# Kernel tuning notes

Hardware: AMD Instinct MI355X
Metric: run time of the kernel (lower is better)

Reference implementation:

```python
import jax, jax.numpy as jnp
import numpy as np

D_MODEL = 2048
NUM_EXPERTS = 64
TOP_K = 2


def setup_inputs() -> dict:
    key = jax.random.key(0)
    kx, kw, kb = jax.random.split(key, 3)
    x = jax.random.normal(kx, (4, 4096, D_MODEL), dtype=jnp.float32)
    # nn.Linear default init: U(-1/sqrt(fan_in), 1/sqrt(fan_in))
    bound = 1.0 / np.sqrt(D_MODEL)
    W = jax.random.uniform(kw, (NUM_EXPERTS, D_MODEL), dtype=jnp.float32, minval=-bound, maxval=bound)
    b = jax.random.uniform(kb, (NUM_EXPERTS,), dtype=jnp.float32, minval=-bound, maxval=bound)
    return {"x": x, "W": W, "b": b}


def reference(x, W, b):
    # Router logits: [B, S, E]
    logits = jnp.einsum("bsd,ed->bse", x, W) + b
    # Top-k over expert dim
    max_k, max_k_index = jax.lax.top_k(logits, TOP_K)  # [B,S,K]
    # Scatter top-k logits into -inf background (equivalent to torch scatter
    # since scattered values are the logits themselves at those indices)
    mask = jnp.any(
        max_k_index[..., None] == jnp.arange(NUM_EXPERTS), axis=-2
    )  # [B,S,E] bool
    sparse = jnp.where(mask, logits, -jnp.inf)
    sf = jax.nn.softmax(sparse, axis=-1)
    return sf, max_k_index
```

## Files before the change

kernel.cpp:

```cpp
#include <hip/hip_runtime.h>
#include <hip/hip_bf16.h>
#include <math.h>

constexpr int D      = 2048;
constexpr int NE     = 64;
constexpr int TOKENS = 16384;
constexpr int TPB    = 64;
constexpr int NBLK   = TOKENS / TPB;
constexpr int NWAVE  = 8;
constexpr int KSLICE = D / NWAVE;
constexpr int KC     = 32;
constexpr int NKC    = KSLICE / KC;
constexpr int PAD    = 66;
constexpr int NM     = TPB / 16;

typedef __attribute__((ext_vector_type(8))) short bf16x8;
typedef __attribute__((ext_vector_type(4))) float f32x4;

static __device__ inline unsigned short f2bf_u(float x) {
  __hip_bfloat16 h = __float2bfloat16(x);
  unsigned short u; __builtin_memcpy(&u, &h, 2); return u;
}
static __device__ inline float bfu2f(unsigned short u) {
  __hip_bfloat16 h; __builtin_memcpy(&h, &u, 2);
  return __bfloat162float(h);
}

static __device__ inline void cvt_hilo(const float* f, bf16x8& hi, bf16x8& lo) {
#pragma unroll
  for (int j = 0; j < 8; ++j) {
    unsigned short h = f2bf_u(f[j]);
    float hf = bfu2f(h);
    unsigned short lw = f2bf_u(f[j] - hf);
    hi[j] = (short)h;
    lo[j] = (short)lw;
  }
}

__global__ __launch_bounds__(256)
void prep_w(const float* __restrict__ W, unsigned short* __restrict__ Whi,
            unsigned short* __restrict__ Wlo) {
  const int i = (blockIdx.x * 256 + threadIdx.x) * 4;
  float4 v = *reinterpret_cast<const float4*>(W + i);
  float f[4] = {v.x, v.y, v.z, v.w};
#pragma unroll
  for (int j = 0; j < 4; ++j) {
    unsigned short h = f2bf_u(f[j]);
    float hf = bfu2f(h);
    Whi[i + j] = h;
    Wlo[i + j] = f2bf_u(f[j] - hf);
  }
}

__global__ __launch_bounds__(512, 2)
void router_main(const float* __restrict__ X,
                 const unsigned short* __restrict__ Whi,
                 const unsigned short* __restrict__ Wlo,
                 const float* __restrict__ bias,
                 float* __restrict__ out) {
  __shared__ float red[4][TPB][PAD];
  __shared__ int   i1s[TPB], i2s[TPB];
  __shared__ float p1s[TPB], p2s[TPB];

  const int t  = threadIdx.x;
  const int w  = t >> 6;
  const int l  = t & 63;
  const int lm = l & 15;
  const int lk = l >> 4;
  const int tile = (blockIdx.x & 7) * (NBLK / 8) + (blockIdx.x >> 3);
  const int tok0 = tile * TPB;

  f32x4 acc[NM][4];
#pragma unroll
  for (int m = 0; m < NM; ++m)
#pragma unroll
    for (int n = 0; n < 4; ++n) acc[m][n] = (f32x4){0.f, 0.f, 0.f, 0.f};

  const unsigned short* whp = Whi + (size_t)lm * D + w * KSLICE + lk * 8;
  const unsigned short* wlp = Wlo + (size_t)lm * D + w * KSLICE + lk * 8;
  const float* xr[NM];
#pragma unroll
  for (int m = 0; m < NM; ++m)
    xr[m] = X + (size_t)(tok0 + m * 16 + lm) * D + w * KSLICE + lk * 8;

  float4 c0[NM], c1[NM];
#pragma unroll
  for (int m = 0; m < NM; ++m) {
    c0[m] = *reinterpret_cast<const float4*>(xr[m]);
    c1[m] = *reinterpret_cast<const float4*>(xr[m] + 4);
  }

#pragma unroll
  for (int kc = 0; kc < NKC; ++kc) {
    const int ko = kc * KC;

    bf16x8 bh[4], bl[4];
#pragma unroll
    for (int n = 0; n < 4; ++n) {
      bh[n] = *reinterpret_cast<const bf16x8*>(whp + (size_t)n * 16 * D + ko);
      bl[n] = *reinterpret_cast<const bf16x8*>(wlp + (size_t)n * 16 * D + ko);
    }

    float4 n0[NM], n1[NM];
    if (kc < NKC - 1) {
#pragma unroll
      for (int m = 0; m < NM; ++m) {
        n0[m] = *reinterpret_cast<const float4*>(xr[m] + (kc + 1) * KC);
        n1[m] = *reinterpret_cast<const float4*>(xr[m] + (kc + 1) * KC + 4);
      }
    }

#pragma unroll
    for (int m = 0; m < NM; ++m) {
      float f[8];
      *reinterpret_cast<float4*>(&f[0]) = c0[m];
      *reinterpret_cast<float4*>(&f[4]) = c1[m];
      bf16x8 ah, al;
      cvt_hilo(f, ah, al);
#pragma unroll
      for (int n = 0; n < 4; ++n) {
        acc[m][n] = __builtin_amdgcn_mfma_f32_16x16x32_bf16(ah, bh[n], acc[m][n], 0, 0, 0);
        acc[m][n] = __builtin_amdgcn_mfma_f32_16x16x32_bf16(ah, bl[n], acc[m][n], 0, 0, 0);
        acc[m][n] = __builtin_amdgcn_mfma_f32_16x16x32_bf16(al, bh[n], acc[m][n], 0, 0, 0);
        acc[m][n] = __builtin_amdgcn_mfma_f32_16x16x32_bf16(al, bl[n], acc[m][n], 0, 0, 0);
      }
    }
    if (kc < NKC - 1) {
#pragma unroll
      for (int m = 0; m < NM; ++m) { c0[m] = n0[m]; c1[m] = n1[m]; }
    }
  }

  const int rtok = t >> 3;
  const int re0  = (t & 7) * 8;
  float s[8];

  if (w < 4) {
#pragma unroll
    for (int m = 0; m < NM; ++m)
#pragma unroll
      for (int n = 0; n < 4; ++n)
#pragma unroll
        for (int j = 0; j < 4; ++j)
          red[w][m * 16 + lk * 4 + j][n * 16 + lm] = acc[m][n][j];
  }
  __syncthreads();
#pragma unroll
  for (int q = 0; q < 8; ++q) {
    const int e = re0 + q;
    float v = bias[e];
#pragma unroll
    for (int ww = 0; ww < 4; ++ww) v += red[ww][rtok][e];
    s[q] = v;
  }
  __syncthreads();
  if (w >= 4) {
#pragma unroll
    for (int m = 0; m < NM; ++m)
#pragma unroll
      for (int n = 0; n < 4; ++n)
#pragma unroll
        for (int j = 0; j < 4; ++j)
          red[w - 4][m * 16 + lk * 4 + j][n * 16 + lm] = acc[m][n][j];
  }
  __syncthreads();
#pragma unroll
  for (int q = 0; q < 8; ++q) {
    const int e = re0 + q;
    float v = s[q];
#pragma unroll
    for (int ww = 0; ww < 4; ++ww) v += red[ww][rtok][e];
    red[0][rtok][e] = v;
  }
  __syncthreads();

  if (t < TPB) {
    float m1 = -INFINITY, m2 = -INFINITY;
    int j1 = 0, j2 = 0;
    for (int e = 0; e < NE; ++e) {
      const float v = red[0][t][e];
      if (v > m1) { m2 = m1; j2 = j1; m1 = v; j1 = e; }
      else if (v > m2) { m2 = v; j2 = e; }
    }
    const float e2  = expf(m2 - m1);
    const float inv = 1.0f / (1.0f + e2);
    i1s[t] = j1; i2s[t] = j2;
    p1s[t] = inv; p2s[t] = e2 * inv;
    float* oidx = out + (size_t)TOKENS * NE + (size_t)(tok0 + t) * 2;
    oidx[0] = (float)j1;
    oidx[1] = (float)j2;
  }
  __syncthreads();

  {
    const int tok = t >> 3;
    const int e0  = (t & 7) * 8;
    const int j1 = i1s[tok], j2 = i2s[tok];
    const float pa = p1s[tok], pb2 = p2s[tok];
    float vv[8];
#pragma unroll
    for (int q = 0; q < 8; ++q) {
      const int e = e0 + q;
      vv[q] = (e == j1) ? pa : ((e == j2) ? pb2 : 0.f);
    }
    float* obase = out + (size_t)(tok0 + tok) * NE + e0;
    *reinterpret_cast<float4*>(obase)     = make_float4(vv[0], vv[1], vv[2], vv[3]);
    *reinterpret_cast<float4*>(obase + 4) = make_float4(vv[4], vv[5], vv[6], vv[7]);
  }
}

extern "C" void kernel_launch(void* const* d_in, const int* in_sizes, int n_in,
                              void* d_out, int out_size, void* d_ws, size_t ws_size,
                              hipStream_t stream) {
  const float* X = (const float*)d_in[0];
  const float* W = (const float*)d_in[1];
  const float* B = (const float*)d_in[2];
  float* out = (float*)d_out;

  unsigned short* Whi = (unsigned short*)d_ws;
  unsigned short* Wlo = Whi + (size_t)NE * D;

  prep_w<<<dim3(NE * D / (256 * 4)), dim3(256), 0, stream>>>(W, Whi, Wlo);
  router_main<<<dim3(NBLK), dim3(512), 0, stream>>>(X, Whi, Wlo, B, out);
}
```

Baseline: 47.84 us.

## Split token tiles across two wave groups with 1024-thread blocks

Doubles the block to 16 waves, with each group of 8 K-slice waves handling half of the 64 tokens (two 16-row tiles instead of four). This halves per-thread accumulator and prefetch registers so more waves can be resident, aiming to hide X load latency better. In exchange, each W fragment is now loaded by twice as many waves, adding cache traffic, and the larger blocks may reduce scheduling flexibility.

After: 60.72 us. 26.9% more time.

```diff
diff --git a/kernel.cpp b/kernel.cpp
--- a/kernel.cpp
+++ b/kernel.cpp
@@ -12,7 +12,6 @@
 constexpr int KC     = 32;
 constexpr int NKC    = KSLICE / KC;
 constexpr int PAD    = 66;
-constexpr int NM     = TPB / 16;
 
 typedef __attribute__((ext_vector_type(8))) short bf16x8;
 typedef __attribute__((ext_vector_type(4))) float f32x4;
@@ -52,7 +51,7 @@
   }
 }
 
-__global__ __launch_bounds__(512, 2)
+__global__ __launch_bounds__(1024, 4)
 void router_main(const float* __restrict__ X,
                  const unsigned short* __restrict__ Whi,
                  const unsigned short* __restrict__ Wlo,
@@ -63,29 +62,31 @@
   __shared__ float p1s[TPB], p2s[TPB];
 
   const int t  = threadIdx.x;
-  const int w  = t >> 6;
+  const int wv = t >> 6;
+  const int w  = wv & 7;
+  const int h  = wv >> 3;
   const int l  = t & 63;
   const int lm = l & 15;
   const int lk = l >> 4;
   const int tile = (blockIdx.x & 7) * (NBLK / 8) + (blockIdx.x >> 3);
   const int tok0 = tile * TPB;
 
-  f32x4 acc[NM][4];
-#pragma unroll
-  for (int m = 0; m < NM; ++m)
+  f32x4 acc[2][4];
+#pragma unroll
+  for (int m = 0; m < 2; ++m)
 #pragma unroll
     for (int n = 0; n < 4; ++n) acc[m][n] = (f32x4){0.f, 0.f, 0.f, 0.f};
 
   const unsigned short* whp = Whi + (size_t)lm * D + w * KSLICE + lk * 8;
   const unsigned short* wlp = Wlo + (size_t)lm * D + w * KSLICE + lk * 8;
-  const float* xr[NM];
-#pragma unroll
-  for (int m = 0; m < NM; ++m)
-    xr[m] = X + (size_t)(tok0 + m * 16 + lm) * D + w * KSLICE + lk * 8;
-
-  float4 c0[NM], c1[NM];
-#pragma unroll
-  for (int m = 0; m < NM; ++m) {
+  const float* xr[2];
+#pragma unroll
+  for (int m = 0; m < 2; ++m)
+    xr[m] = X + (size_t)(tok0 + (h * 2 + m) * 16 + lm) * D + w * KSLICE + lk * 8;
+
+  float4 c0[2], c1[2];
+#pragma unroll
+  for (int m = 0; m < 2; ++m) {
     c0[m] = *reinterpret_cast<const float4*>(xr[m]);
     c1[m] = *reinterpret_cast<const float4*>(xr[m] + 4);
   }
@@ -101,17 +102,17 @@
       bl[n] = *reinterpret_cast<const bf16x8*>(wlp + (size_t)n * 16 * D + ko);
     }
 
-    float4 n0[NM], n1[NM];
+    float4 n0[2], n1[2];
     if (kc < NKC - 1) {
 #pragma unroll
-      for (int m = 0; m < NM; ++m) {
+      for (int m = 0; m < 2; ++m) {
         n0[m] = *reinterpret_cast<const float4*>(xr[m] + (kc + 1) * KC);
         n1[m] = *reinterpret_cast<const float4*>(xr[m] + (kc + 1) * KC + 4);
       }
     }
 
 #pragma unroll
-    for (int m = 0; m < NM; ++m) {
+    for (int m = 0; m < 2; ++m) {
       float f[8];
       *reinterpret_cast<float4*>(&f[0]) = c0[m];
       *reinterpret_cast<float4*>(&f[4]) = c1[m];
@@ -127,26 +128,26 @@
     }
     if (kc < NKC - 1) {
 #pragma unroll
-      for (int m = 0; m < NM; ++m) { c0[m] = n0[m]; c1[m] = n1[m]; }
-    }
-  }
-
-  const int rtok = t >> 3;
-  const int re0  = (t & 7) * 8;
-  float s[8];
+      for (int m = 0; m < 2; ++m) { c0[m] = n0[m]; c1[m] = n1[m]; }
+    }
+  }
+
+  const int rtok = t >> 4;
+  const int re0  = (t & 15) * 4;
+  float s[4];
 
   if (w < 4) {
 #pragma unroll
-    for (int m = 0; m < NM; ++m)
+    for (int m = 0; m < 2; ++m)
 #pragma unroll
       for (int n = 0; n < 4; ++n)
 #pragma unroll
         for (int j = 0; j < 4; ++j)
-          red[w][m * 16 + lk * 4 + j][n * 16 + lm] = acc[m][n][j];
-  }
-  __syncthreads();
-#pragma unroll
-  for (int q = 0; q < 8; ++q) {
+          red[w][(h * 2 + m) * 16 + lk * 4 + j][n * 16 + lm] = acc[m][n][j];
+  }
+  __syncthreads();
+#pragma unroll
+  for (int q = 0; q < 4; ++q) {
     const int e = re0 + q;
     float v = bias[e];
 #pragma unroll
@@ -156,16 +157,16 @@
   __syncthreads();
   if (w >= 4) {
 #pragma unroll
-    for (int m = 0; m < NM; ++m)
+    for (int m = 0; m < 2; ++m)
 #pragma unroll
       for (int n = 0; n < 4; ++n)
 #pragma unroll
         for (int j = 0; j < 4; ++j)
-          red[w - 4][m * 16 + lk * 4 + j][n * 16 + lm] = acc[m][n][j];
-  }
-  __syncthreads();
-#pragma unroll
-  for (int q = 0; q < 8; ++q) {
+          red[w - 4][(h * 2 + m) * 16 + lk * 4 + j][n * 16 + lm] = acc[m][n][j];
+  }
+  __syncthreads();
+#pragma unroll
+  for (int q = 0; q < 4; ++q) {
     const int e = re0 + q;
     float v = s[q];
 #pragma unroll
@@ -193,19 +194,18 @@
   __syncthreads();
 
   {
-    const int tok = t >> 3;
-    const int e0  = (t & 7) * 8;
+    const int tok = t >> 4;
+    const int e0  = (t & 15) * 4;
     const int j1 = i1s[tok], j2 = i2s[tok];
     const float pa = p1s[tok], pb2 = p2s[tok];
-    float vv[8];
-#pragma unroll
-    for (int q = 0; q < 8; ++q) {
+    float vv[4];
+#pragma unroll
+    for (int q = 0; q < 4; ++q) {
       const int e = e0 + q;
       vv[q] = (e == j1) ? pa : ((e == j2) ? pb2 : 0.f);
     }
-    float* obase = out + (size_t)(tok0 + tok) * NE + e0;
-    *reinterpret_cast<float4*>(obase)     = make_float4(vv[0], vv[1], vv[2], vv[3]);
-    *reinterpret_cast<float4*>(obase + 4) = make_float4(vv[4], vv[5], vv[6], vv[7]);
+    *reinterpret_cast<float4*>(out + (size_t)(tok0 + tok) * NE + e0) =
+        make_float4(vv[0], vv[1], vv[2], vv[3]);
   }
 }
 
@@ -221,5 +221,5 @@
   unsigned short* Wlo = Whi + (size_t)NE * D;
 
   prep_w<<<dim3(NE * D / (256 * 4)), dim3(256), 0, stream>>>(W, Whi, Wlo);
-  router_main<<<dim3(NBLK), dim3(512), 0, stream>>>(X, Whi, Wlo, B, out);
-}
+  router_main<<<dim3(NBLK), dim3(1024), 0, stream>>>(X, Whi, Wlo, B, out);
+}
```

## Stage X tiles through double-buffered swizzled LDS and split waves over M/N

Applied to the files above, without the earlier changes.

Before, each of eight waves read its own K slice of X straight from global memory and covered all 64 tokens and 64 experts. Now the block loads one 256-wide K slice of X for all 64 tokens into double-buffered, XOR-swizzled shared memory. Each wave computes a 16x32 output sub-tile over that slice and partial sums are reduced through LDS every slice. This is meant to give coalesced X loads and overlap the next slice's load with the MFMAs. In exchange it adds 128KB of LDS, which likely drops occupancy to one block per CU, plus two barriers per slice.

Result: slower. 115.6 us (+141.6%).

```diff
diff --git a/kernel.cpp b/kernel.cpp
--- a/kernel.cpp
+++ b/kernel.cpp
@@ -7,12 +7,11 @@
 constexpr int TOKENS = 16384;
 constexpr int TPB    = 64;
 constexpr int NBLK   = TOKENS / TPB;
-constexpr int NWAVE  = 8;
-constexpr int KSLICE = D / NWAVE;
+constexpr int NSL    = 8;
+constexpr int KSLICE = D / NSL;
 constexpr int KC     = 32;
 constexpr int NKC    = KSLICE / KC;
 constexpr int PAD    = 66;
-constexpr int NM     = TPB / 16;
 
 typedef __attribute__((ext_vector_type(8))) short bf16x8;
 typedef __attribute__((ext_vector_type(4))) float f32x4;
@@ -58,127 +57,118 @@
                  const unsigned short* __restrict__ Wlo,
                  const float* __restrict__ bias,
                  float* __restrict__ out) {
-  __shared__ float red[4][TPB][PAD];
+  __shared__ __align__(16) float xbuf[2][TPB * KSLICE / 1];
+  __shared__ float red[TPB][PAD];
   __shared__ int   i1s[TPB], i2s[TPB];
   __shared__ float p1s[TPB], p2s[TPB];
 
   const int t  = threadIdx.x;
-  const int w  = t >> 6;
+  const int wv = t >> 6;
+  const int mh = wv >> 1;
+  const int nh = wv & 1;
   const int l  = t & 63;
   const int lm = l & 15;
   const int lk = l >> 4;
   const int tile = (blockIdx.x & 7) * (NBLK / 8) + (blockIdx.x >> 3);
   const int tok0 = tile * TPB;
 
-  f32x4 acc[NM][4];
-#pragma unroll
-  for (int m = 0; m < NM; ++m)
-#pragma unroll
-    for (int n = 0; n < 4; ++n) acc[m][n] = (f32x4){0.f, 0.f, 0.f, 0.f};
-
-  const unsigned short* whp = Whi + (size_t)lm * D + w * KSLICE + lk * 8;
-  const unsigned short* wlp = Wlo + (size_t)lm * D + w * KSLICE + lk * 8;
-  const float* xr[NM];
-#pragma unroll
-  for (int m = 0; m < NM; ++m)
-    xr[m] = X + (size_t)(tok0 + m * 16 + lm) * D + w * KSLICE + lk * 8;
-
-  float4 c0[NM], c1[NM];
-#pragma unroll
-  for (int m = 0; m < NM; ++m) {
-    c0[m] = *reinterpret_cast<const float4*>(xr[m]);
-    c1[m] = *reinterpret_cast<const float4*>(xr[m] + 4);
-  }
-
-#pragma unroll
-  for (int kc = 0; kc < NKC; ++kc) {
-    const int ko = kc * KC;
-
-    bf16x8 bh[4], bl[4];
-#pragma unroll
-    for (int n = 0; n < 4; ++n) {
-      bh[n] = *reinterpret_cast<const bf16x8*>(whp + (size_t)n * 16 * D + ko);
-      bl[n] = *reinterpret_cast<const bf16x8*>(wlp + (size_t)n * 16 * D + ko);
-    }
-
-    float4 n0[NM], n1[NM];
-    if (kc < NKC - 1) {
-#pragma unroll
-      for (int m = 0; m < NM; ++m) {
-        n0[m] = *reinterpret_cast<const float4*>(xr[m] + (kc + 1) * KC);
-        n1[m] = *reinterpret_cast<const float4*>(xr[m] + (kc + 1) * KC + 4);
+  const unsigned short* whp[2];
+#pragma unroll
+  for (int n = 0; n < 2; ++n)
+    whp[n] = Whi + (size_t)((nh * 2 + n) * 16 + lm) * D + lk * 8;
+
+  float4 g[8];
+  auto issue_loads = [&](int ss) {
+#pragma unroll
+    for (int j = 0; j < 8; ++j) {
+      const int r = wv * 8 + j;
+      const char* rowsrc = reinterpret_cast<const char*>(
+          X + (size_t)(tok0 + r) * D + ss * KSLICE);
+      g[j] = *reinterpret_cast<const float4*>(rowsrc + ((l * 16) ^ ((r & 7) << 4)));
+    }
+  };
+  auto write_lds = [&](int nb) {
+#pragma unroll
+    for (int j = 0; j < 8; ++j) {
+      const int r = wv * 8 + j;
+      char* rowdst = reinterpret_cast<char*>(&xbuf[nb][r * KSLICE]);
+      *reinterpret_cast<float4*>(rowdst + l * 16) = g[j];
+    }
+  };
+
+  issue_loads(0);
+  write_lds(0);
+  __syncthreads();
+
+  const int rtok = t >> 3;
+  const int re0  = (t & 7) * 8;
+  float sreg[8];
+#pragma unroll
+  for (int q = 0; q < 8; ++q) sreg[q] = bias[re0 + q];
+
+  int cb = 0;
+#pragma unroll 1
+  for (int s = 0; s < NSL; ++s) {
+    if (s < NSL - 1) issue_loads(s + 1);
+
+    f32x4 acc[2];
+#pragma unroll
+    for (int n = 0; n < 2; ++n) acc[n] = (f32x4){0.f, 0.f, 0.f, 0.f};
+
+    const int row = mh * 16 + lm;
+    const int sw  = (row & 7) << 4;
+    const char* rb = reinterpret_cast<const char*>(&xbuf[cb][row * KSLICE]);
+
+#pragma unroll
+    for (int kc = 0; kc < NKC; ++kc) {
+      bf16x8 bh[2], bl[2];
+#pragma unroll
+      for (int n = 0; n < 2; ++n) {
+        const unsigned short* wp = whp[n] + (size_t)s * KSLICE + kc * KC;
+        bh[n] = *reinterpret_cast<const bf16x8*>(wp);
+        bl[n] = *reinterpret_cast<const bf16x8*>(wp + (size_t)NE * D);
       }
-    }
-
-#pragma unroll
-    for (int m = 0; m < NM; ++m) {
+      const int b = kc * 128 + lk * 32;
       float f[8];
-      *reinterpret_cast<float4*>(&f[0]) = c0[m];
-      *reinterpret_cast<float4*>(&f[4]) = c1[m];
+      *reinterpret_cast<float4*>(&f[0]) =
+          *reinterpret_cast<const float4*>(rb + (b ^ sw));
+      *reinterpret_cast<float4*>(&f[4]) =
+          *reinterpret_cast<const float4*>(rb + ((b + 16) ^ sw));
       bf16x8 ah, al;
       cvt_hilo(f, ah, al);
 #pragma unroll
-      for (int n = 0; n < 4; ++n) {
-        acc[m][n] = __builtin_amdgcn_mfma_f32_16x16x32_bf16(ah, bh[n], acc[m][n], 0, 0, 0);
-        acc[m][n] = __builtin_amdgcn_mfma_f32_16x16x32_bf16(ah, bl[n], acc[m][n], 0, 0, 0);
-        acc[m][n] = __builtin_amdgcn_mfma_f32_16x16x32_bf16(al, bh[n], acc[m][n], 0, 0, 0);
-        acc[m][n] = __builtin_amdgcn_mfma_f32_16x16x32_bf16(al, bl[n], acc[m][n], 0, 0, 0);
+      for (int n = 0; n < 2; ++n) {
+        acc[n] = __builtin_amdgcn_mfma_f32_16x16x32_bf16(ah, bh[n], acc[n], 0, 0, 0);
+        acc[n] = __builtin_amdgcn_mfma_f32_16x16x32_bf16(ah, bl[n], acc[n], 0, 0, 0);
+        acc[n] = __builtin_amdgcn_mfma_f32_16x16x32_bf16(al, bh[n], acc[n], 0, 0, 0);
+        acc[n] = __builtin_amdgcn_mfma_f32_16x16x32_bf16(al, bl[n], acc[n], 0, 0, 0);
       }
     }
-    if (kc < NKC - 1) {
-#pragma unroll
-      for (int m = 0; m < NM; ++m) { c0[m] = n0[m]; c1[m] = n1[m]; }
-    }
-  }
-
-  const int rtok = t >> 3;
-  const int re0  = (t & 7) * 8;
-  float s[8];
-
-  if (w < 4) {
-#pragma unroll
-    for (int m = 0; m < NM; ++m)
-#pragma unroll
-      for (int n = 0; n < 4; ++n)
-#pragma unroll
-        for (int j = 0; j < 4; ++j)
-          red[w][m * 16 + lk * 4 + j][n * 16 + lm] = acc[m][n][j];
-  }
-  __syncthreads();
-#pragma unroll
-  for (int q = 0; q < 8; ++q) {
-    const int e = re0 + q;
-    float v = bias[e];
-#pragma unroll
-    for (int ww = 0; ww < 4; ++ww) v += red[ww][rtok][e];
-    s[q] = v;
-  }
-  __syncthreads();
-  if (w >= 4) {
-#pragma unroll
-    for (int m = 0; m < NM; ++m)
-#pragma unroll
-      for (int n = 0; n < 4; ++n)
-#pragma unroll
-        for (int j = 0; j < 4; ++j)
-          red[w - 4][m * 16 + lk * 4 + j][n * 16 + lm] = acc[m][n][j];
-  }
-  __syncthreads();
-#pragma unroll
-  for (int q = 0; q < 8; ++q) {
-    const int e = re0 + q;
-    float v = s[q];
-#pragma unroll
-    for (int ww = 0; ww < 4; ++ww) v += red[ww][rtok][e];
-    red[0][rtok][e] = v;
-  }
+
+    if (s < NSL - 1) write_lds(cb ^ 1);
+
+#pragma unroll
+    for (int n = 0; n < 2; ++n)
+#pragma unroll
+      for (int j = 0; j < 4; ++j)
+        red[mh * 16 + lk * 4 + j][(nh * 2 + n) * 16 + lm] = acc[n][j];
+    __syncthreads();
+
+#pragma unroll
+    for (int q = 0; q < 8; ++q) sreg[q] += red[rtok][re0 + q];
+    __syncthreads();
+    cb ^= 1;
+  }
+
+#pragma unroll
+  for (int q = 0; q < 8; ++q) red[rtok][re0 + q] = sreg[q];
   __syncthreads();
 
   if (t < TPB) {
     float m1 = -INFINITY, m2 = -INFINITY;
     int j1 = 0, j2 = 0;
     for (int e = 0; e < NE; ++e) {
-      const float v = red[0][t][e];
+      const float v = red[t][e];
       if (v > m1) { m2 = m1; j2 = j1; m1 = v; j1 = e; }
       else if (v > m2) { m2 = v; j2 = e; }
     }
```
